# Performance work log

Hardware: AMD Instinct MI355X
Metric: run time of the kernel (lower is better)

Reference implementation:

```python
import jax, jax.numpy as jnp
import numpy as np

N = 20000   # nodes per frame
T = 16      # frames
E = 320000  # edges per frame
C = 128     # in_channels
H = 128     # hidden_channels
P = 100000  # decode pairs


def setup_inputs() -> dict:
    key = jax.random.key(0)
    ks = jax.random.split(key, 12)
    s = 1.0 / np.sqrt(H)
    return {
        "x_seq": jax.random.normal(ks[0], (T, N, C), jnp.float32),
        "edge_index": jax.random.randint(ks[1], (T, 2, E), 0, N, jnp.int32),
        "edge_pairs": jax.random.randint(ks[2], (2, P), 0, N, jnp.int32),
        "W1": jax.random.normal(ks[3], (C, H), jnp.float32) * s,
        "b1": jnp.zeros((H,), jnp.float32),
        "W2": jax.random.normal(ks[4], (H, H), jnp.float32) * s,
        "b2": jnp.zeros((H,), jnp.float32),
        "W3": jax.random.normal(ks[5], (H, H), jnp.float32) * s,
        "b3": jnp.zeros((H,), jnp.float32),
        "w_ih": jax.random.normal(ks[6], (3 * H, H), jnp.float32) * s,
        "w_hh": jax.random.normal(ks[7], (3 * H, H), jnp.float32) * s,
        "b_ih": jnp.zeros((3 * H,), jnp.float32),
        "b_hh": jnp.zeros((3 * H,), jnp.float32),
    }


def _gcn(x, src, dst, W, b):
    # PyG GCNConv: h = x @ W; add self-loops; D^{-1/2}(A+I)D^{-1/2} aggregation; + b
    h = x @ W                                   # [N, H]
    ones = jnp.ones(src.shape[0], x.dtype)
    deg = jax.ops.segment_sum(ones, dst, num_segments=N) + 1.0  # self-loop included
    dinv = jax.lax.rsqrt(deg)
    norm = dinv[src] * dinv[dst]                # [E]
    agg = jax.ops.segment_sum(h[src] * norm[:, None], dst, num_segments=N)
    agg = agg + h * (dinv * dinv)[:, None]      # self-loop message (norm = 1/deg)
    return agg + b


def reference(x_seq, edge_index, edge_pairs, W1, b1, W2, b2, W3, b3,
              w_ih, w_hh, b_ih, b_hh):
    def frame(_, inp):
        x, ei = inp
        src, dst = ei[0], ei[1]
        h = jax.nn.relu(_gcn(x, src, dst, W1, b1))
        h = jax.nn.relu(_gcn(h, src, dst, W2, b2))
        h = _gcn(h, src, dst, W3, b3)
        return None, h

    _, feats = jax.lax.scan(frame, None, (x_seq, edge_index))  # [T, N, H]

    # single-layer torch GRU over time; only final hidden state needed
    def gru_step(hprev, x_t):
        gi = x_t @ w_ih.T + b_ih                # [N, 3H]
        gh = hprev @ w_hh.T + b_hh
        i_r, i_z, i_n = jnp.split(gi, 3, axis=1)
        h_r, h_z, h_n = jnp.split(gh, 3, axis=1)
        r = jax.nn.sigmoid(i_r + h_r)
        z = jax.nn.sigmoid(i_z + h_z)
        n = jnp.tanh(i_n + r * h_n)
        h_new = (1.0 - z) * n + z * hprev
        return h_new, None

    h0 = jnp.zeros((N, H), x_seq.dtype)
    h_last, _ = jax.lax.scan(gru_step, h0, feats)  # [N, H]

    zs = h_last[edge_pairs[0]]                  # [P, H]
    zd = h_last[edge_pairs[1]]
    return jnp.sum(zs * zd, axis=1)             # [P]
```

## Files before the change

### kernel.cpp

```cpp
#include <hip/hip_runtime.h>
#include <hip/hip_bf16.h>

#define NN 20000
#define TT 16
#define EE 320000
#define CC 128
#define HH 128
#define PP 100000
#define QN (NN / 4)

typedef float  f32x4  __attribute__((ext_vector_type(4)));
typedef unsigned short ushort8v __attribute__((ext_vector_type(8)));
typedef _Float16 h2v __attribute__((ext_vector_type(2)));
typedef _Float16 h4v __attribute__((ext_vector_type(4)));
typedef _Float16 f16x8 __attribute__((ext_vector_type(8)));


__global__ void hist_all_k(const int* __restrict__ edge_index, int* __restrict__ cnt_all) {
    int b = blockIdx.x;
    int f = b & 15, chunk = b >> 4;
    const int* dst = edge_index + (size_t)f * 2 * EE + EE;
    int* cnt = cnt_all + f * NN;
    int base = chunk * 1024 + threadIdx.x;
#pragma unroll
    for (int i = 0; i < 4; ++i) {
        int e = base + i * 256;
        if (e < EE) {
            int d = __builtin_nontemporal_load(dst + e);
            atomicAdd(&cnt[d], 1);
        }
    }
}

__global__ __launch_bounds__(1024) void scan_all_k(const int* __restrict__ cnt_all,
                                                   int* __restrict__ offs_all,
                                                   float* __restrict__ dinv_all,
                                                   int* __restrict__ cursor_all) {
    __shared__ int part[1024];
    int f = blockIdx.x;
    const int* cnt = cnt_all + f * NN;
    int* offs = offs_all + f * (NN + 1);
    int t = threadIdx.x;
    int base = t * 20;
    int vals[20];
    int s = 0;
#pragma unroll
    for (int i = 0; i < 20; ++i) {
        int idx = base + i;
        int v = (idx < NN) ? cnt[idx] : 0;
        vals[i] = v; s += v;
    }
    part[t] = s;
    __syncthreads();
    for (int off = 1; off < 1024; off <<= 1) {
        int v = (t >= off) ? part[t - off] : 0;
        __syncthreads();
        part[t] += v;
        __syncthreads();
    }
    int run = part[t] - s;
#pragma unroll
    for (int i = 0; i < 20; ++i) {
        int idx = base + i;
        if (idx < NN) {
            offs[idx] = run;
            cursor_all[f * NN + idx] = f * EE + run;
            dinv_all[f * NN + idx] = rsqrtf((float)vals[i] + 1.0f);
            run += vals[i];
        }
    }
    if (t == 0) offs[NN] = EE;
}

__global__ void fill_all_k(const int* __restrict__ edge_index,
                           int* __restrict__ cursor_all,
                           unsigned short* __restrict__ csr_all) {
    int b = blockIdx.x;
    int f = b & 15, chunk = b >> 4;
    const int* src = edge_index + (size_t)f * 2 * EE;
    const int* dst = src + EE;
    int* cur = cursor_all + f * NN;
    int base = chunk * 1024 + threadIdx.x;
#pragma unroll
    for (int i = 0; i < 4; ++i) {
        int e = base + i * 256;
        if (e < EE) {
            int d = __builtin_nontemporal_load(dst + e);
            int s = __builtin_nontemporal_load(src + e);
            int pos = atomicAdd(&cur[d], 1);
            csr_all[pos] = (unsigned short)s;
        }
    }
}

__global__ void wprep_t_k(const float* __restrict__ W,
                          _Float16* __restrict__ oh,
                          _Float16* __restrict__ ol) {
    int i = blockIdx.x * blockDim.x + threadIdx.x;
    if (i >= 128 * 128) return;
    int n = i >> 7, k = i & 127;
    float v = W[k * 128 + n];
    _Float16 h = (_Float16)v;
    oh[i] = h;
    ol[i] = (_Float16)(v - (float)h);
}

__global__ void wprep_d_k(const float* __restrict__ w,
                          _Float16* __restrict__ oh,
                          _Float16* __restrict__ ol, int n) {
    int i = blockIdx.x * blockDim.x + threadIdx.x;
    if (i >= n) return;
    float v = w[i];
    _Float16 h = (_Float16)v;
    oh[i] = h;
    ol[i] = (_Float16)(v - (float)h);
}

__global__ __launch_bounds__(256) void scale_k(const float* __restrict__ x,
                                               const float* __restrict__ dinv_all,
                                               _Float16* __restrict__ g) {
    int idx = blockIdx.x * blockDim.x + threadIdx.x;
    int row = idx >> 5, q = idx & 31;
    const f32x4* xp = (const f32x4*)(x + (size_t)row * 128 + q * 4);
    f32x4 v = __builtin_nontemporal_load(xp);
    float d = dinv_all[row];
    h4v o;
    o.x = (_Float16)(v.x * d); o.y = (_Float16)(v.y * d);
    o.z = (_Float16)(v.z * d); o.w = (_Float16)(v.w * d);
    *(h4v*)(g + (size_t)row * 128 + q * 4) = o;
}

__global__ __launch_bounds__(128) void agg_half_k(const _Float16* __restrict__ g,
                                                  const unsigned short* __restrict__ csr_all,
                                                  const int* __restrict__ offs_all,
                                                  _Float16* __restrict__ a) {
    int b = blockIdx.x;
    int xcd = b & 7;
    int r1 = b >> 3;
    int grp = r1 % QN;
    int pass = r1 / QN;
    int f = xcd + ((pass & 1) << 3);
    int hoff = (pass >> 1) * 64;
    int t = threadIdx.x;
    int node = grp * 4 + (t >> 5);
    int lane = t & 31;
    const int* offs = offs_all + f * (NN + 1);
    const unsigned short* csr = csr_all + (size_t)f * EE;
    const _Float16* gf = g + (size_t)f * NN * HH + hoff + lane * 2;
    int beg = offs[node], end = offs[node + 1];
    float a0 = 0.f, a1 = 0.f;
    int e = beg;
    for (; e + 3 < end; e += 4) {
        int s0 = csr[e], s1 = csr[e + 1], s2 = csr[e + 2], s3 = csr[e + 3];
        h2v v0 = *(const h2v*)(gf + (size_t)s0 * HH);
        h2v v1 = *(const h2v*)(gf + (size_t)s1 * HH);
        h2v v2 = *(const h2v*)(gf + (size_t)s2 * HH);
        h2v v3 = *(const h2v*)(gf + (size_t)s3 * HH);
        a0 += ((float)v0.x + (float)v1.x) + ((float)v2.x + (float)v3.x);
        a1 += ((float)v0.y + (float)v1.y) + ((float)v2.y + (float)v3.y);
    }
    for (; e < end; ++e) {
        h2v v = *(const h2v*)(gf + (size_t)csr[e] * HH);
        a0 += (float)v.x; a1 += (float)v.y;
    }
    h2v vs = *(const h2v*)(gf + (size_t)node * HH);
    a0 += (float)vs.x; a1 += (float)vs.y;
    h2v r; r.x = (_Float16)a0; r.y = (_Float16)a1;
    *(h2v*)(a + ((size_t)f * NN + node) * HH + hoff + lane * 2) = r;
}

__global__ __launch_bounds__(256) void gemm_f16(const _Float16* __restrict__ A,
                                                const _Float16* __restrict__ Bh,
                                                const _Float16* __restrict__ Bl,
                                                _Float16* __restrict__ out,
                                                const float* __restrict__ rowscale,
                                                const float* __restrict__ bias,
                                                int M, int NC, int relu, int postscale) {
    __shared__ _Float16 As[64 * 72], Bhs[64 * 72], Bls[64 * 72];
    int t = threadIdx.x;
    int b = blockIdx.x;
    int xcd = b & 7, k = b >> 3;
    int row_t = xcd + ((k >> 1) << 3);
    int col_t = k & 1;
    int row0 = row_t * 64, col0 = col_t * 64;
    int w = t >> 6, lane = t & 63;
    int wm = (w & 1) * 32, wn = (w >> 1) * 32;
    int lm = lane & 15, lq = lane >> 4;
    f32x4 acc[2][2] = {};

    for (int ks = 0; ks < 2; ++ks) {
        if (ks) __syncthreads();
#pragma unroll
        for (int p = 0; p < 2; ++p) {
            int s = t + p * 256;
            int r = s >> 3, c8 = s & 7;
            int gr = row0 + r;
            ushort8v va = {};
            if (gr < M)
                va = *(const ushort8v*)(A + (size_t)gr * 128 + ks * 64 + c8 * 8);
            *(ushort8v*)&As[r * 72 + c8 * 8] = va;
            *(ushort8v*)&Bhs[r * 72 + c8 * 8] =
                *(const ushort8v*)(Bh + (size_t)(col0 + r) * 128 + ks * 64 + c8 * 8);
            *(ushort8v*)&Bls[r * 72 + c8 * 8] =
                *(const ushort8v*)(Bl + (size_t)(col0 + r) * 128 + ks * 64 + c8 * 8);
        }
        __syncthreads();
#pragma unroll
        for (int q = 0; q < 2; ++q) {
            int ko = q * 32 + lq * 8;
            f16x8 av[2], bh[2], bl[2];
#pragma unroll
            for (int i = 0; i < 2; ++i)
                av[i] = *(const f16x8*)&As[(wm + i * 16 + lm) * 72 + ko];
#pragma unroll
            for (int j = 0; j < 2; ++j) {
                bh[j] = *(const f16x8*)&Bhs[(wn + j * 16 + lm) * 72 + ko];
                bl[j] = *(const f16x8*)&Bls[(wn + j * 16 + lm) * 72 + ko];
            }
#pragma unroll
            for (int i = 0; i < 2; ++i)
#pragma unroll
                for (int j = 0; j < 2; ++j) {
                    acc[i][j] = __builtin_amdgcn_mfma_f32_16x16x32_f16(av[i], bh[j], acc[i][j], 0, 0, 0);
                    acc[i][j] = __builtin_amdgcn_mfma_f32_16x16x32_f16(av[i], bl[j], acc[i][j], 0, 0, 0);
                }
        }
    }
#pragma unroll
    for (int i = 0; i < 2; ++i)
#pragma unroll
        for (int reg = 0; reg < 4; ++reg) {
            int gr = row0 + wm + i * 16 + lq * 4 + reg;
            if (gr < M) {
                float sc = rowscale ? rowscale[gr] : 1.0f;
#pragma unroll
                for (int j = 0; j < 2; ++j) {
                    int col = col0 + wn + j * 16 + lm;
                    float v = acc[i][j][reg];
                    if (rowscale) v *= sc;
                    v += bias[col];
                    if (relu) v = fmaxf(v, 0.f);
                    if (postscale) v *= sc;
                    out[(size_t)gr * NC + col] = (_Float16)v;
                }
            }
        }
}

__global__ __launch_bounds__(512, 2) void gru_all_k(const _Float16* __restrict__ F,
                                                    const _Float16* __restrict__ wihh,
                                                    const _Float16* __restrict__ wihl,
                                                    const _Float16* __restrict__ whhh,
                                                    const _Float16* __restrict__ whhl,
                                                    const float* __restrict__ b_ih,
                                                    const float* __restrict__ b_hh,
                                                    float* __restrict__ hgru) {
    __shared__ float hs[128][132];
    __shared__ _Float16 Fs[128][136];
    int t = threadIdx.x;
    int row0 = blockIdx.x * 128;
    for (int s = t; s < 128 * 132; s += 512) ((float*)hs)[s] = 0.f;

    int w = t >> 6, lane = t & 63;
    int lm = lane & 15, lq = lane >> 4;
    int h_idx = w * 16 + lm;
    float bri = b_ih[h_idx], bzi = b_ih[h_idx + 128], bni = b_ih[h_idx + 256];
    float brh = b_hh[h_idx], bzh = b_hh[h_idx + 128], bnh = b_hh[h_idx + 256];
    size_t wbase = (size_t)h_idx * 128 + lq * 8;

    for (int tt = 0; tt < TT; ++tt) {
        __syncthreads();
        const _Float16* Ft = F + ((size_t)tt * NN + row0) * 128;
#pragma unroll
        for (int i2 = 0; i2 < 4; ++i2) {
            int s = t + i2 * 512;
            int r = s >> 4, v = s & 15;
            ushort8v val = {};
            if (row0 + r < NN) val = *(const ushort8v*)(Ft + (size_t)r * 128 + v * 8);
            *(ushort8v*)&Fs[r][v * 8] = val;
        }
        __syncthreads();

        f32x4 accr[8], accz[8], accni[8], accnh[8];
#pragma unroll
        for (int i = 0; i < 8; ++i) {
            accr[i] = (f32x4){0.f, 0.f, 0.f, 0.f};
            accz[i] = (f32x4){0.f, 0.f, 0.f, 0.f};
            accni[i] = (f32x4){0.f, 0.f, 0.f, 0.f};
            accnh[i] = (f32x4){0.f, 0.f, 0.f, 0.f};
        }

#pragma unroll
        for (int q = 0; q < 4; ++q) {
            f16x8 af[8];
#pragma unroll
            for (int i = 0; i < 8; ++i)
                af[i] = *(const f16x8*)&Fs[i * 16 + lm][q * 32 + lq * 8];
            size_t o = wbase + q * 32;
            f16x8 brhh = *(const f16x8*)(wihh + o);
            f16x8 brll = *(const f16x8*)(wihl + o);
            f16x8 bzhh = *(const f16x8*)(wihh + o + 16384);
            f16x8 bzll = *(const f16x8*)(wihl + o + 16384);
            f16x8 bnhh = *(const f16x8*)(wihh + o + 32768);
            f16x8 bnll = *(const f16x8*)(wihl + o + 32768);
#pragma unroll
            for (int i = 0; i < 8; ++i) {
                accr[i]  = __builtin_amdgcn_mfma_f32_16x16x32_f16(af[i], brhh, accr[i], 0, 0, 0);
                accr[i]  = __builtin_amdgcn_mfma_f32_16x16x32_f16(af[i], brll, accr[i], 0, 0, 0);
                accz[i]  = __builtin_amdgcn_mfma_f32_16x16x32_f16(af[i], bzhh, accz[i], 0, 0, 0);
                accz[i]  = __builtin_amdgcn_mfma_f32_16x16x32_f16(af[i], bzll, accz[i], 0, 0, 0);
                accni[i] = __builtin_amdgcn_mfma_f32_16x16x32_f16(af[i], bnhh, accni[i], 0, 0, 0);
                accni[i] = __builtin_amdgcn_mfma_f32_16x16x32_f16(af[i], bnll, accni[i], 0, 0, 0);
            }
        }

#pragma unroll
        for (int q = 0; q < 4; ++q) {
            f16x8 ah[8], al[8];
#pragma unroll
            for (int i = 0; i < 8; ++i) {
                const float* hp = &hs[i * 16 + lm][q * 32 + lq * 8];
#pragma unroll
                for (int e = 0; e < 8; ++e) {
                    float f = hp[e];
                    _Float16 hh = (_Float16)f;
                    ah[i][e] = hh;
                    al[i][e] = (_Float16)(f - (float)hh);
                }
            }
            size_t o = wbase + q * 32;
            f16x8 brhh = *(const f16x8*)(whhh + o);
            f16x8 brll = *(const f16x8*)(whhl + o);
            f16x8 bzhh = *(const f16x8*)(whhh + o + 16384);
            f16x8 bzll = *(const f16x8*)(whhl + o + 16384);
            f16x8 bnhh = *(const f16x8*)(whhh + o + 32768);
            f16x8 bnll = *(const f16x8*)(whhl + o + 32768);
#pragma unroll
            for (int i = 0; i < 8; ++i) {
                accr[i]  = __builtin_amdgcn_mfma_f32_16x16x32_f16(ah[i], brhh, accr[i], 0, 0, 0);
                accr[i]  = __builtin_amdgcn_mfma_f32_16x16x32_f16(ah[i], brll, accr[i], 0, 0, 0);
                accr[i]  = __builtin_amdgcn_mfma_f32_16x16x32_f16(al[i], brhh, accr[i], 0, 0, 0);
                accz[i]  = __builtin_amdgcn_mfma_f32_16x16x32_f16(ah[i], bzhh, accz[i], 0, 0, 0);
                accz[i]  = __builtin_amdgcn_mfma_f32_16x16x32_f16(ah[i], bzll, accz[i], 0, 0, 0);
                accz[i]  = __builtin_amdgcn_mfma_f32_16x16x32_f16(al[i], bzhh, accz[i], 0, 0, 0);
                accnh[i] = __builtin_amdgcn_mfma_f32_16x16x32_f16(ah[i], bnhh, accnh[i], 0, 0, 0);
                accnh[i] = __builtin_amdgcn_mfma_f32_16x16x32_f16(ah[i], bnll, accnh[i], 0, 0, 0);
                accnh[i] = __builtin_amdgcn_mfma_f32_16x16x32_f16(al[i], bnhh, accnh[i], 0, 0, 0);
            }
        }

        float hnew[8][4];
#pragma unroll
        for (int i = 0; i < 8; ++i)
#pragma unroll
            for (int reg = 0; reg < 4; ++reg) {
                int row_l = i * 16 + lq * 4 + reg;
                float hp = hs[row_l][h_idx];
                float r = 1.f / (1.f + __expf(-(accr[i][reg] + bri + brh)));
                float z = 1.f / (1.f + __expf(-(accz[i][reg] + bzi + bzh)));
                float nv = tanhf(accni[i][reg] + bni + r * (accnh[i][reg] + bnh));
                hnew[i][reg] = (1.f - z) * nv + z * hp;
            }
        __syncthreads();
#pragma unroll
        for (int i = 0; i < 8; ++i)
#pragma unroll
            for (int reg = 0; reg < 4; ++reg) {
                int row_l = i * 16 + lq * 4 + reg;
                hs[row_l][h_idx] = hnew[i][reg];
                if (tt == TT - 1 && row0 + row_l < NN)
                    hgru[(size_t)(row0 + row_l) * 128 + h_idx] = hnew[i][reg];
            }
    }
}

__global__ __launch_bounds__(256) void decode_k(const float* __restrict__ hgru,
                                                const int* __restrict__ pairs,
                                                float* __restrict__ out) {
    int gid = blockIdx.x * blockDim.x + threadIdx.x;
    int w = gid >> 6;
    int lane = threadIdx.x & 63;
    if (w >= PP) return;
    int s = pairs[w], d = pairs[PP + w];
    const float* zs = hgru + (size_t)s * HH;
    const float* zd = hgru + (size_t)d * HH;
    float acc = zs[lane] * zd[lane] + zs[lane + 64] * zd[lane + 64];
#pragma unroll
    for (int off = 32; off > 0; off >>= 1) acc += __shfl_down(acc, off);
    if (lane == 0) out[w] = acc;
}

static inline size_t align256(size_t x) { return (x + 255) & ~(size_t)255; }

extern "C" void kernel_launch(void* const* d_in, const int* in_sizes, int n_in,
                              void* d_out, int out_size, void* d_ws, size_t ws_size,
                              hipStream_t stream) {
    const float* x_seq      = (const float*)d_in[0];
    const int*   edge_index = (const int*)d_in[1];
    const int*   edge_pairs = (const int*)d_in[2];
    const float* W1 = (const float*)d_in[3];
    const float* b1 = (const float*)d_in[4];
    const float* W2 = (const float*)d_in[5];
    const float* b2 = (const float*)d_in[6];
    const float* W3 = (const float*)d_in[7];
    const float* b3 = (const float*)d_in[8];
    const float* w_ih = (const float*)d_in[9];
    const float* w_hh = (const float*)d_in[10];
    const float* b_ih = (const float*)d_in[11];
    const float* b_hh = (const float*)d_in[12];

    const size_t MALL = (size_t)TT * NN;

    char* p = (char*)d_ws;
    int*   cnt_all    = (int*)p;   p += align256(MALL * sizeof(int));
    int*   offs_all   = (int*)p;   p += align256((size_t)TT * (NN + 1) * sizeof(int));
    int*   cursor_all = (int*)p;   p += align256(MALL * sizeof(int));
    float* dinv_all   = (float*)p; p += align256(MALL * sizeof(float));
    unsigned short* csr_all = (unsigned short*)p; p += align256((size_t)TT * EE * sizeof(unsigned short));
    _Float16* g   = (_Float16*)p;  p += align256(MALL * HH * sizeof(_Float16));
    _Float16* a   = (_Float16*)p;  p += align256(MALL * HH * sizeof(_Float16));
    _Float16* F   = (_Float16*)p;  p += align256(MALL * HH * sizeof(_Float16));
    float* hgru = (float*)p;       p += align256((size_t)NN * HH * sizeof(float));
    _Float16* W1h = (_Float16*)p; p += align256(128 * 128 * 2);
    _Float16* W1l = (_Float16*)p; p += align256(128 * 128 * 2);
    _Float16* W2h = (_Float16*)p; p += align256(128 * 128 * 2);
    _Float16* W2l = (_Float16*)p; p += align256(128 * 128 * 2);
    _Float16* W3h = (_Float16*)p; p += align256(128 * 128 * 2);
    _Float16* W3l = (_Float16*)p; p += align256(128 * 128 * 2);
    _Float16* wihh = (_Float16*)p; p += align256(384 * 128 * 2);
    _Float16* wihl = (_Float16*)p; p += align256(384 * 128 * 2);
    _Float16* whhh = (_Float16*)p; p += align256(384 * 128 * 2);
    _Float16* whhl = (_Float16*)p; p += align256(384 * 128 * 2);

    hipMemsetAsync(cnt_all, 0, MALL * sizeof(int), stream);

    wprep_t_k<<<64, 256, 0, stream>>>(W1, W1h, W1l);
    wprep_t_k<<<64, 256, 0, stream>>>(W2, W2h, W2l);
    wprep_t_k<<<64, 256, 0, stream>>>(W3, W3h, W3l);
    wprep_d_k<<<192, 256, 0, stream>>>(w_ih, wihh, wihl, 384 * 128);
    wprep_d_k<<<192, 256, 0, stream>>>(w_hh, whhh, whhl, 384 * 128);

    int ge = ((EE + 1023) / 1024) * TT;
    hist_all_k<<<ge, 256, 0, stream>>>(edge_index, cnt_all);
    scan_all_k<<<TT, 1024, 0, stream>>>(cnt_all, offs_all, dinv_all, cursor_all);
    fill_all_k<<<ge, 256, 0, stream>>>(edge_index, cursor_all, csr_all);

    scale_k<<<(int)(MALL * 32 / 256), 256, 0, stream>>>(x_seq, dinv_all, g);

    int gagg = 8 * QN * 4;
    int ggemm = 2 * (int)(MALL / 64);

    agg_half_k<<<gagg, 128, 0, stream>>>(g, csr_all, offs_all, a);
    gemm_f16<<<ggemm, 256, 0, stream>>>(a, W1h, W1l, g, dinv_all, b1, (int)MALL, 128, 1, 1);
    agg_half_k<<<gagg, 128, 0, stream>>>(g, csr_all, offs_all, a);
    gemm_f16<<<ggemm, 256, 0, stream>>>(a, W2h, W2l, g, dinv_all, b2, (int)MALL, 128, 1, 1);
    agg_half_k<<<gagg, 128, 0, stream>>>(g, csr_all, offs_all, a);
    gemm_f16<<<ggemm, 256, 0, stream>>>(a, W3h, W3l, F, dinv_all, b3, (int)MALL, 128, 0, 0);

    int gru_blocks = (NN + 127) / 128;
    gru_all_k<<<gru_blocks, 512, 0, stream>>>(F, wihh, wihl, whhh, whhl,
                                              b_ih, b_hh, hgru);

    decode_k<<<(PP * 64 + 255) / 256, 256, 0, stream>>>(hgru, edge_pairs, (float*)d_out);
}
```

Before: 1.800 ms.

## Restructure GRU kernel with 64-row tiles, split-f16 hidden state, direct F loads

The GRU kernel now processes 64 rows per block instead of 128, which halves the accumulator registers and lets launch bounds request 4 blocks per CU. The hidden state is kept in shared memory as packed hi/lo f16 pairs with an XOR swizzle, so the per-step float-to-split conversion and bank conflicts are avoided. F tiles are read straight from global memory into MFMA operands, which drops the shared staging buffer and one barrier per step. The trade-offs are small recomputation of hp from hi+lo with a possible tiny precision change, and weight fragments reloaded across twice as many blocks.

```diff
diff --git a/kernel.cpp b/kernel.cpp
--- a/kernel.cpp
+++ b/kernel.cpp
@@ -11,9 +11,12 @@
 
 typedef float  f32x4  __attribute__((ext_vector_type(4)));
 typedef unsigned short ushort8v __attribute__((ext_vector_type(8)));
+typedef unsigned u32x4 __attribute__((ext_vector_type(4)));
 typedef _Float16 h2v __attribute__((ext_vector_type(2)));
 typedef _Float16 h4v __attribute__((ext_vector_type(4)));
 typedef _Float16 f16x8 __attribute__((ext_vector_type(8)));
+
+union pk16 { unsigned u; _Float16 h[2]; };
 
 
 __global__ void hist_all_k(const int* __restrict__ edge_index, int* __restrict__ cnt_all) {
@@ -247,7 +250,7 @@
         }
 }
 
-__global__ __launch_bounds__(512, 2) void gru_all_k(const _Float16* __restrict__ F,
+__global__ __launch_bounds__(512, 4) void gru_all_k(const _Float16* __restrict__ F,
                                                     const _Float16* __restrict__ wihh,
                                                     const _Float16* __restrict__ wihl,
                                                     const _Float16* __restrict__ whhh,
@@ -255,35 +258,33 @@
                                                     const float* __restrict__ b_ih,
                                                     const float* __restrict__ b_hh,
                                                     float* __restrict__ hgru) {
-    __shared__ float hs[128][132];
-    __shared__ _Float16 Fs[128][136];
+    __shared__ unsigned hs2[64 * 132];
     int t = threadIdx.x;
-    int row0 = blockIdx.x * 128;
-    for (int s = t; s < 128 * 132; s += 512) ((float*)hs)[s] = 0.f;
+    int row0 = blockIdx.x * 64;
+    for (int s = t; s < 64 * 132; s += 512) hs2[s] = 0u;
 
     int w = t >> 6, lane = t & 63;
     int lm = lane & 15, lq = lane >> 4;
     int h_idx = w * 16 + lm;
-    float bri = b_ih[h_idx], bzi = b_ih[h_idx + 128], bni = b_ih[h_idx + 256];
-    float brh = b_hh[h_idx], bzh = b_hh[h_idx + 128], bnh = b_hh[h_idx + 256];
+    float bsr = b_ih[h_idx] + b_hh[h_idx];
+    float bsz = b_ih[h_idx + 128] + b_hh[h_idx + 128];
+    float bni = b_ih[h_idx + 256];
+    float bnh = b_hh[h_idx + 256];
     size_t wbase = (size_t)h_idx * 128 + lq * 8;
+    const _Float16* Fb = F + (size_t)(row0 + lm) * 128 + lq * 8;
+    bool rowok[4];
+#pragma unroll
+    for (int i = 0; i < 4; ++i) rowok[i] = (row0 + i * 16 + lm) < NN;
+
+    char* hsb = (char*)hs2;
 
     for (int tt = 0; tt < TT; ++tt) {
         __syncthreads();
-        const _Float16* Ft = F + ((size_t)tt * NN + row0) * 128;
-#pragma unroll
-        for (int i2 = 0; i2 < 4; ++i2) {
-            int s = t + i2 * 512;
-            int r = s >> 4, v = s & 15;
-            ushort8v val = {};
-            if (row0 + r < NN) val = *(const ushort8v*)(Ft + (size_t)r * 128 + v * 8);
-            *(ushort8v*)&Fs[r][v * 8] = val;
-        }
-        __syncthreads();
-
-        f32x4 accr[8], accz[8], accni[8], accnh[8];
-#pragma unroll
-        for (int i = 0; i < 8; ++i) {
+        const _Float16* Ft = Fb + (size_t)tt * NN * 128;
+
+        f32x4 accr[4], accz[4], accni[4], accnh[4];
+#pragma unroll
+        for (int i = 0; i < 4; ++i) {
             accr[i] = (f32x4){0.f, 0.f, 0.f, 0.f};
             accz[i] = (f32x4){0.f, 0.f, 0.f, 0.f};
             accni[i] = (f32x4){0.f, 0.f, 0.f, 0.f};
@@ -292,84 +293,89 @@
 
 #pragma unroll
         for (int q = 0; q < 4; ++q) {
-            f16x8 af[8];
-#pragma unroll
-            for (int i = 0; i < 8; ++i)
-                af[i] = *(const f16x8*)&Fs[i * 16 + lm][q * 32 + lq * 8];
             size_t o = wbase + q * 32;
-            f16x8 brhh = *(const f16x8*)(wihh + o);
-            f16x8 brll = *(const f16x8*)(wihl + o);
-            f16x8 bzhh = *(const f16x8*)(wihh + o + 16384);
-            f16x8 bzll = *(const f16x8*)(wihl + o + 16384);
-            f16x8 bnhh = *(const f16x8*)(wihh + o + 32768);
-            f16x8 bnll = *(const f16x8*)(wihl + o + 32768);
-#pragma unroll
-            for (int i = 0; i < 8; ++i) {
-                accr[i]  = __builtin_amdgcn_mfma_f32_16x16x32_f16(af[i], brhh, accr[i], 0, 0, 0);
-                accr[i]  = __builtin_amdgcn_mfma_f32_16x16x32_f16(af[i], brll, accr[i], 0, 0, 0);
-                accz[i]  = __builtin_amdgcn_mfma_f32_16x16x32_f16(af[i], bzhh, accz[i], 0, 0, 0);
-                accz[i]  = __builtin_amdgcn_mfma_f32_16x16x32_f16(af[i], bzll, accz[i], 0, 0, 0);
-                accni[i] = __builtin_amdgcn_mfma_f32_16x16x32_f16(af[i], bnhh, accni[i], 0, 0, 0);
-                accni[i] = __builtin_amdgcn_mfma_f32_16x16x32_f16(af[i], bnll, accni[i], 0, 0, 0);
+            f16x8 wr_h = *(const f16x8*)(wihh + o);
+            f16x8 wr_l = *(const f16x8*)(wihl + o);
+            f16x8 wz_h = *(const f16x8*)(wihh + o + 16384);
+            f16x8 wz_l = *(const f16x8*)(wihl + o + 16384);
+            f16x8 wn_h = *(const f16x8*)(wihh + o + 32768);
+            f16x8 wn_l = *(const f16x8*)(wihl + o + 32768);
+            f16x8 af[4];
+#pragma unroll
+            for (int i = 0; i < 4; ++i)
+                af[i] = rowok[i] ? *(const f16x8*)(Ft + (size_t)i * 2048 + q * 32)
+                                 : (f16x8){};
+#pragma unroll
+            for (int i = 0; i < 4; ++i) {
+                accr[i]  = __builtin_amdgcn_mfma_f32_16x16x32_f16(af[i], wr_h, accr[i], 0, 0, 0);
+                accr[i]  = __builtin_amdgcn_mfma_f32_16x16x32_f16(af[i], wr_l, accr[i], 0, 0, 0);
+                accz[i]  = __builtin_amdgcn_mfma_f32_16x16x32_f16(af[i], wz_h, accz[i], 0, 0, 0);
+                accz[i]  = __builtin_amdgcn_mfma_f32_16x16x32_f16(af[i], wz_l, accz[i], 0, 0, 0);
+                accni[i] = __builtin_amdgcn_mfma_f32_16x16x32_f16(af[i], wn_h, accni[i], 0, 0, 0);
+                accni[i] = __builtin_amdgcn_mfma_f32_16x16x32_f16(af[i], wn_l, accni[i], 0, 0, 0);
             }
         }
 
 #pragma unroll
         for (int q = 0; q < 4; ++q) {
-            f16x8 ah[8], al[8];
-#pragma unroll
-            for (int i = 0; i < 8; ++i) {
-                const float* hp = &hs[i * 16 + lm][q * 32 + lq * 8];
-#pragma unroll
-                for (int e = 0; e < 8; ++e) {
-                    float f = hp[e];
-                    _Float16 hh = (_Float16)f;
-                    ah[i][e] = hh;
-                    al[i][e] = (_Float16)(f - (float)hh);
+            size_t o = wbase + q * 32;
+            f16x8 wr_h = *(const f16x8*)(whhh + o);
+            f16x8 wr_l = *(const f16x8*)(whhl + o);
+            f16x8 wz_h = *(const f16x8*)(whhh + o + 16384);
+            f16x8 wz_l = *(const f16x8*)(whhl + o + 16384);
+            f16x8 wn_h = *(const f16x8*)(whhh + o + 32768);
+            f16x8 wn_l = *(const f16x8*)(whhl + o + 32768);
+#pragma unroll
+            for (int i = 0; i < 4; ++i) {
+                int row = i * 16 + lm;
+                int c0 = (q * 32 + lq * 8) * 4;
+                int c1 = c0 + 16;
+                int sw = (row & 7) << 4;
+                u32x4 v0 = *(const u32x4*)(hsb + row * 528 + (c0 ^ sw));
+                u32x4 v1 = *(const u32x4*)(hsb + row * 528 + (c1 ^ sw));
+                f16x8 ah, al;
+#pragma unroll
+                for (int e = 0; e < 4; ++e) {
+                    pk16 c; c.u = v0[e]; ah[e] = c.h[0]; al[e] = c.h[1];
+                    pk16 d; d.u = v1[e]; ah[e + 4] = d.h[0]; al[e + 4] = d.h[1];
                 }
-            }
-            size_t o = wbase + q * 32;
-            f16x8 brhh = *(const f16x8*)(whhh + o);
-            f16x8 brll = *(const f16x8*)(whhl + o);
-            f16x8 bzhh = *(const f16x8*)(whhh + o + 16384);
-            f16x8 bzll = *(const f16x8*)(whhl + o + 16384);
-            f16x8 bnhh = *(const f16x8*)(whhh + o + 32768);
-            f16x8 bnll = *(const f16x8*)(whhl + o + 32768);
-#pragma unroll
-            for (int i = 0; i < 8; ++i) {
-                accr[i]  = __builtin_amdgcn_mfma_f32_16x16x32_f16(ah[i], brhh, accr[i], 0, 0, 0);
-                accr[i]  = __builtin_amdgcn_mfma_f32_16x16x32_f16(ah[i], brll, accr[i], 0, 0, 0);
-                accr[i]  = __builtin_amdgcn_mfma_f32_16x16x32_f16(al[i], brhh, accr[i], 0, 0, 0);
-                accz[i]  = __builtin_amdgcn_mfma_f32_16x16x32_f16(ah[i], bzhh, accz[i], 0, 0, 0);
-                accz[i]  = __builtin_amdgcn_mfma_f32_16x16x32_f16(ah[i], bzll, accz[i], 0, 0, 0);
-                accz[i]  = __builtin_amdgcn_mfma_f32_16x16x32_f16(al[i], bzhh, accz[i], 0, 0, 0);
-                accnh[i] = __builtin_amdgcn_mfma_f32_16x16x32_f16(ah[i], bnhh, accnh[i], 0, 0, 0);
-                accnh[i] = __builtin_amdgcn_mfma_f32_16x16x32_f16(ah[i], bnll, accnh[i], 0, 0, 0);
-                accnh[i] = __builtin_amdgcn_mfma_f32_16x16x32_f16(al[i], bnhh, accnh[i], 0, 0, 0);
-            }
-        }
-
-        float hnew[8][4];
-#pragma unroll
-        for (int i = 0; i < 8; ++i)
+                accr[i]  = __builtin_amdgcn_mfma_f32_16x16x32_f16(ah, wr_h, accr[i], 0, 0, 0);
+                accr[i]  = __builtin_amdgcn_mfma_f32_16x16x32_f16(ah, wr_l, accr[i], 0, 0, 0);
+                accr[i]  = __builtin_amdgcn_mfma_f32_16x16x32_f16(al, wr_h, accr[i], 0, 0, 0);
+                accz[i]  = __builtin_amdgcn_mfma_f32_16x16x32_f16(ah, wz_h, accz[i], 0, 0, 0);
+                accz[i]  = __builtin_amdgcn_mfma_f32_16x16x32_f16(ah, wz_l, accz[i], 0, 0, 0);
+                accz[i]  = __builtin_amdgcn_mfma_f32_16x16x32_f16(al, wz_h, accz[i], 0, 0, 0);
+                accnh[i] = __builtin_amdgcn_mfma_f32_16x16x32_f16(ah, wn_h, accnh[i], 0, 0, 0);
+                accnh[i] = __builtin_amdgcn_mfma_f32_16x16x32_f16(ah, wn_l, accnh[i], 0, 0, 0);
+                accnh[i] = __builtin_amdgcn_mfma_f32_16x16x32_f16(al, wn_h, accnh[i], 0, 0, 0);
+            }
+        }
+
+#pragma unroll
+        for (int i = 0; i < 4; ++i)
 #pragma unroll
             for (int reg = 0; reg < 4; ++reg) {
                 int row_l = i * 16 + lq * 4 + reg;
-                float hp = hs[row_l][h_idx];
-                float r = 1.f / (1.f + __expf(-(accr[i][reg] + bri + brh)));
-                float z = 1.f / (1.f + __expf(-(accz[i][reg] + bzi + bzh)));
+                pk16 c;
+                c.u = *(const unsigned*)(hsb + row_l * 528 + ((h_idx * 4) ^ ((row_l & 7) << 4)));
+                float hp = (float)c.h[0] + (float)c.h[1];
+                float r = 1.f / (1.f + __expf(-(accr[i][reg] + bsr)));
+                float z = 1.f / (1.f + __expf(-(accz[i][reg] + bsz)));
                 float nv = tanhf(accni[i][reg] + bni + r * (accnh[i][reg] + bnh));
-                hnew[i][reg] = (1.f - z) * nv + z * hp;
+                accr[i][reg] = (1.f - z) * nv + z * hp;
             }
         __syncthreads();
 #pragma unroll
-        for (int i = 0; i < 8; ++i)
+        for (int i = 0; i < 4; ++i)
 #pragma unroll
             for (int reg = 0; reg < 4; ++reg) {
                 int row_l = i * 16 + lq * 4 + reg;
-                hs[row_l][h_idx] = hnew[i][reg];
+                float hv = accr[i][reg];
+                _Float16 hi = (_Float16)hv;
+                pk16 c; c.h[0] = hi; c.h[1] = (_Float16)(hv - (float)hi);
+                *(unsigned*)(hsb + row_l * 528 + ((h_idx * 4) ^ ((row_l & 7) << 4))) = c.u;
                 if (tt == TT - 1 && row0 + row_l < NN)
-                    hgru[(size_t)(row0 + row_l) * 128 + h_idx] = hnew[i][reg];
+                    hgru[(size_t)(row0 + row_l) * 128 + h_idx] = hv;
             }
     }
 }
@@ -457,7 +463,7 @@
     agg_half_k<<<gagg, 128, 0, stream>>>(g, csr_all, offs_all, a);
     gemm_f16<<<ggemm, 256, 0, stream>>>(a, W3h, W3l, F, dinv_all, b3, (int)MALL, 128, 0, 0);
 
-    int gru_blocks = (NN + 127) / 128;
+    int gru_blocks = (NN + 63) / 64;
     gru_all_k<<<gru_blocks, 512, 0, stream>>>(F, wihh, wihl, whhh, whhl,
                                               b_ih, b_hh, hgru);
 
```

New measurement: 2.049 ms. 13.9% more time.
